# Kernel optimization log

Measured on AMD Instinct MI355X. Metric: run time of the kernel, lower is better.

## Reference

```python
import jax, jax.numpy as jnp
import numpy as np

N, F, E, LIN, C, B = 16384, 500, 128, 128, 10, 4096
P_EDGE = 0.002  # ~32 avg degree


def _l2norm(x):
    # F.normalize(dim=1), eps=1e-12
    n = jnp.linalg.norm(x, axis=1, keepdims=True)
    return x / jnp.maximum(n, 1e-12)


def setup_inputs() -> dict:
    key = jax.random.key(0)
    ks = jax.random.split(key, 10)
    adj = (jax.random.uniform(ks[0], (N, N)) < P_EDGE).astype(jnp.float32)
    idx = jnp.arange(N)
    adj = adj.at[idx, idx].set(1.0)  # self-loops guarantee degree >= 1
    data = jax.random.normal(ks[1], (N, F), dtype=jnp.float32)
    nodes = jax.random.randint(ks[2], (B,), 0, N)
    # Encoder 1: Linear(2F -> E); Encoder 2: Linear(2E -> E); classifier heads
    W1 = jax.random.normal(ks[3], (E, 2 * F), dtype=jnp.float32) * 0.03
    b1 = jnp.zeros((E,), jnp.float32)
    W2 = jax.random.normal(ks[4], (E, 2 * E), dtype=jnp.float32) * 0.06
    b2 = jnp.zeros((E,), jnp.float32)
    Wl1 = jax.random.normal(ks[5], (LIN, E), dtype=jnp.float32) * 0.08
    bl1 = jnp.zeros((LIN,), jnp.float32)
    Wl2 = jax.random.normal(ks[6], (C, LIN), dtype=jnp.float32) * 0.12
    bl2 = jnp.zeros((C,), jnp.float32)
    return {"nodes": nodes, "adj": adj, "data": data,
            "W1": W1, "b1": b1, "W2": W2, "b2": b2,
            "Wl1": Wl1, "bl1": bl1, "Wl2": Wl2, "bl2": bl2}


def reference(nodes, adj, data, W1, b1, W2, b2, Wl1, bl1, Wl2, bl2):
    deg = jnp.sum(adj, axis=1, keepdims=True)  # [N,1]
    # Layer 1 (mean aggregator over full neighbor set): computed for all nodes
    neigh1 = (adj @ data) / deg                               # [N,F]
    h1 = jnp.concatenate([data, neigh1], axis=1)              # [N,2F] (self, neigh)
    H1 = _l2norm(jax.nn.relu(h1 @ W1.T + b1))                 # [N,E]
    # Layer 2: only for the queried node batch
    neigh2 = (adj[nodes] @ H1) / deg[nodes]                   # [B,E]
    h2 = jnp.concatenate([H1[nodes], neigh2], axis=1)         # [B,2E]
    H2 = _l2norm(jax.nn.relu(h2 @ W2.T + b2))                 # [B,E]
    x = H2 @ Wl1.T + bl1                                      # [B,LIN]
    x = x @ Wl2.T + bl2                                       # [B,C]
    return jax.nn.softmax(x, axis=1)
```

## Files before the change

kernel.cpp:

```cpp
#include <hip/hip_runtime.h>
#include <math.h>
#include <stddef.h>

#define N_NODES 16384
#define F_DIM   500
#define KP1     512
#define E_DIM   128
#define C_DIM   10
#define B_DIM   4096
#define MAXDEG  128

typedef __attribute__((ext_vector_type(8))) short short8;
typedef __attribute__((ext_vector_type(4))) float f32x4;

__device__ inline unsigned short f2bf(float f) {
    union { float f; unsigned int u; } v; v.f = f;
    unsigned int u = v.u;
    u += 0x7FFFu + ((u >> 16) & 1u);
    return (unsigned short)(u >> 16);
}

__global__ __launch_bounds__(256) void k_cast_data(const float* __restrict__ src,
                                                   unsigned short* __restrict__ dst) {
    int idx = blockIdx.x * 256 + threadIdx.x;
    int i = idx >> 8, k2 = (idx & 255) * 2;
    unsigned short a = 0, b = 0;
    if (k2 < F_DIM) {
        float2 d = *(const float2*)(src + (size_t)i * F_DIM + k2);
        a = f2bf(d.x); b = f2bf(d.y);
    }
    ushort2 o; o.x = a; o.y = b;
    *(ushort2*)(dst + (size_t)i * KP1 + k2) = o;
}

__global__ __launch_bounds__(256) void k_prep_w1b(const float* __restrict__ W1,
                                                  unsigned short* __restrict__ Wt) {
    int idx = blockIdx.x * 256 + threadIdx.x;
    int n = idx >> 9, k = idx & 511;
    float v = (k < F_DIM) ? W1[(size_t)(n & 127) * 1000 + (n >> 7) * F_DIM + k] : 0.0f;
    Wt[idx] = f2bf(v);
}

__global__ __launch_bounds__(256) void k_prep_w2b(const float* __restrict__ W2,
                                                  unsigned short* __restrict__ Wt) {
    int idx = blockIdx.x * 256 + threadIdx.x;
    int n = idx >> 7, k = idx & 127;
    Wt[idx] = f2bf(W2[(size_t)(n & 127) * 256 + (n >> 7) * 128 + k]);
}

__global__ void k_tp(const float* __restrict__ src, float* __restrict__ dst) {
    __shared__ float tile[32][33];
    const int k0 = blockIdx.x * 32;
    const int e0 = blockIdx.y * 32;
    const int tx = threadIdx.x, ty0 = threadIdx.y;
#pragma unroll
    for (int q = 0; q < 4; ++q) {
        int ty = ty0 + q * 8;
        tile[ty][tx] = src[(size_t)(e0 + ty) * 128 + k0 + tx];
    }
    __syncthreads();
#pragma unroll
    for (int q = 0; q < 4; ++q) {
        int ty = ty0 + q * 8;
        dst[(size_t)(k0 + ty) * 128 + e0 + tx] = tile[tx][ty];
    }
}

__global__ __launch_bounds__(256) void k_gemm_mfma(const unsigned short* __restrict__ A,
                                                   const unsigned short* __restrict__ B,
                                                   int K,
                                                   float* __restrict__ Cout) {
    __shared__ unsigned short sA[32 * 40];
    __shared__ unsigned short sB[256 * 40];
    const int tid  = threadIdx.x;
    const int w    = tid >> 6;
    const int lane = tid & 63;
    const int l16  = lane & 15;
    const int quad = lane >> 4;
    const int blockM = blockIdx.x * 32;
    f32x4 acc[2][4] = {};
    const int nchunks = K >> 5;

    for (int c = 0; c < nchunks; ++c) {
        const int k0 = c << 5;
        if (tid < 128) {
            int row = tid >> 2, cc = tid & 3;
            short8 v = *(const short8*)(A + (size_t)(blockM + row) * K + k0 + cc * 8);
            *(short8*)(sA + row * 40 + cc * 8) = v;
        }
#pragma unroll
        for (int q = 0; q < 4; ++q) {
            int idx = tid + 256 * q;
            int row = idx >> 2, cc = idx & 3;
            short8 v = *(const short8*)(B + (size_t)row * K + k0 + cc * 8);
            *(short8*)(sB + row * 40 + cc * 8) = v;
        }
        __syncthreads();
        short8 af[2], bf[4];
#pragma unroll
        for (int mt = 0; mt < 2; ++mt)
            af[mt] = *(const short8*)(sA + (mt * 16 + l16) * 40 + quad * 8);
#pragma unroll
        for (int nt = 0; nt < 4; ++nt)
            bf[nt] = *(const short8*)(sB + (w * 64 + nt * 16 + l16) * 40 + quad * 8);
#pragma unroll
        for (int mt = 0; mt < 2; ++mt)
#pragma unroll
            for (int nt = 0; nt < 4; ++nt)
                acc[mt][nt] = __builtin_amdgcn_mfma_f32_16x16x32_bf16(af[mt], bf[nt], acc[mt][nt], 0, 0, 0);
        __syncthreads();
    }
#pragma unroll
    for (int mt = 0; mt < 2; ++mt)
#pragma unroll
        for (int nt = 0; nt < 4; ++nt) {
            int col = w * 64 + nt * 16 + l16;
#pragma unroll
            for (int r = 0; r < 4; ++r) {
                int row = blockM + mt * 16 + quad * 4 + r;
                Cout[(size_t)row * 256 + col] = acc[mt][nt][r];
            }
        }
}

__global__ __launch_bounds__(256) void k_agg1(const float* __restrict__ adj,
                                              const float* __restrict__ X,
                                              const float* __restrict__ b1,
                                              unsigned short* __restrict__ H1b,
                                              int* __restrict__ nbr,
                                              int* __restrict__ deg) {
    const int i = blockIdx.x;
    const int t = threadIdx.x;
    const float4* row4 = (const float4*)(adj + (size_t)i * N_NODES);
    __shared__ int s_cnt;
    __shared__ int s_idx[MAXDEG];
    __shared__ float s_part[2][128];
    __shared__ float s_w[2];
    if (t == 0) s_cnt = 0;
    __syncthreads();
    float4 v[16];
#pragma unroll
    for (int p = 0; p < 16; ++p) v[p] = row4[p * 256 + t];
#pragma unroll
    for (int p = 0; p < 16; ++p) {
        int col = p * 1024 + t * 4;
        if (v[p].x != 0.f) { int q = atomicAdd(&s_cnt, 1); if (q < MAXDEG) s_idx[q] = col;     }
        if (v[p].y != 0.f) { int q = atomicAdd(&s_cnt, 1); if (q < MAXDEG) s_idx[q] = col + 1; }
        if (v[p].z != 0.f) { int q = atomicAdd(&s_cnt, 1); if (q < MAXDEG) s_idx[q] = col + 2; }
        if (v[p].w != 0.f) { int q = atomicAdd(&s_cnt, 1); if (q < MAXDEG) s_idx[q] = col + 3; }
    }
    __syncthreads();
    int cnt = s_cnt; if (cnt > MAXDEG) cnt = MAXDEG;
    if (t < cnt) nbr[(size_t)i * MAXDEG + t] = s_idx[t];
    if (t == 0) deg[i] = cnt;
    const float inv = 1.0f / (float)cnt;
    const int col = t & 127;
    const int g = t >> 7;
    float acc = 0.f;
    for (int k = g; k < cnt; k += 2)
        acc += X[(size_t)s_idx[k] * 256 + 128 + col];
    s_part[g][col] = acc;
    __syncthreads();
    float vv = 0.f;
    if (t < 128) {
        float tot = s_part[0][t] + s_part[1][t];
        vv = X[(size_t)i * 256 + t] + tot * inv + b1[t];
        vv = fmaxf(vv, 0.f);
        float s = vv * vv;
#pragma unroll
        for (int off = 32; off > 0; off >>= 1) s += __shfl_down(s, off, 64);
        if ((t & 63) == 0) s_w[t >> 6] = s;
    }
    __syncthreads();
    if (t < 128) {
        float denom = fmaxf(sqrtf(s_w[0] + s_w[1]), 1e-12f);
        H1b[(size_t)i * 128 + t] = f2bf(vv / denom);
    }
}

__global__ __launch_bounds__(128) void k_l2head(const int* __restrict__ nodes,
                                                const int* __restrict__ nbr,
                                                const int* __restrict__ deg,
                                                const float* __restrict__ Y,
                                                const float* __restrict__ b2,
                                                const float* __restrict__ Wl1t,
                                                const float* __restrict__ bl1,
                                                const float* __restrict__ Wl2,
                                                const float* __restrict__ bl2,
                                                float* __restrict__ out) {
    const int b = blockIdx.x;
    const int t = threadIdx.x;
    const int n = nodes[b];
    const int cnt = deg[n];
    __shared__ int s_idx[MAXDEG];
    __shared__ float s_h[128];
    __shared__ float s_x[128];
    __shared__ float s_c[C_DIM];
    __shared__ float s_w[2];
    if (t < cnt) s_idx[t] = nbr[(size_t)n * MAXDEG + t];
    __syncthreads();
    float a0 = 0.f, a1 = 0.f;
    int k = 0;
    for (; k + 1 < cnt; k += 2) {
        a0 += Y[(size_t)s_idx[k]     * 256 + 128 + t];
        a1 += Y[(size_t)s_idx[k + 1] * 256 + 128 + t];
    }
    if (k < cnt) a0 += Y[(size_t)s_idx[k] * 256 + 128 + t];
    float vv = Y[(size_t)n * 256 + t] + (a0 + a1) / (float)cnt + b2[t];
    vv = fmaxf(vv, 0.f);
    float s = vv * vv;
#pragma unroll
    for (int off = 32; off > 0; off >>= 1) s += __shfl_down(s, off, 64);
    if ((t & 63) == 0) s_w[t >> 6] = s;
    __syncthreads();
    float denom = fmaxf(sqrtf(s_w[0] + s_w[1]), 1e-12f);
    s_h[t] = vv / denom;
    __syncthreads();
    float x1 = bl1[t];
#pragma unroll 8
    for (int kk = 0; kk < 128; ++kk)
        x1 += Wl1t[kk * 128 + t] * s_h[kk];
    s_x[t] = x1;
    __syncthreads();
    if (t < C_DIM) {
        float l = bl2[t];
        const float* wr = Wl2 + (size_t)t * 128;
        for (int kk = 0; kk < 128; ++kk) l += wr[kk] * s_x[kk];
        s_c[t] = l;
    }
    __syncthreads();
    if (t < C_DIM) {
        float mx = -1e30f;
        for (int c = 0; c < C_DIM; ++c) mx = fmaxf(mx, s_c[c]);
        float se = 0.f;
        for (int c = 0; c < C_DIM; ++c) se += expf(s_c[c] - mx);
        out[(size_t)b * C_DIM + t] = expf(s_c[t] - mx) / se;
    }
}

extern "C" void kernel_launch(void* const* d_in, const int* in_sizes, int n_in,
                              void* d_out, int out_size, void* d_ws, size_t ws_size,
                              hipStream_t stream) {
    const int*   nodes = (const int*)  d_in[0];
    const float* adj   = (const float*)d_in[1];
    const float* data  = (const float*)d_in[2];
    const float* W1    = (const float*)d_in[3];
    const float* b1    = (const float*)d_in[4];
    const float* W2    = (const float*)d_in[5];
    const float* b2    = (const float*)d_in[6];
    const float* Wl1   = (const float*)d_in[7];
    const float* bl1   = (const float*)d_in[8];
    const float* Wl2   = (const float*)d_in[9];
    const float* bl2   = (const float*)d_in[10];
    float* out = (float*)d_out;

    unsigned short* Ab  = (unsigned short*)d_ws;
    unsigned short* Wt1 = Ab  + (size_t)N_NODES * KP1;
    unsigned short* Wt2 = Wt1 + 256 * KP1;
    unsigned short* H1b = Wt2 + 256 * 128;
    float* Wl1t = (float*)(H1b + (size_t)N_NODES * 128);
    float* X    = Wl1t + 128 * 128;
    float* Y    = X    + (size_t)N_NODES * 256;
    int*   nbr  = (int*)(Y + (size_t)N_NODES * 256);
    int*   deg  = nbr + (size_t)N_NODES * MAXDEG;

    k_cast_data<<<N_NODES, 256, 0, stream>>>(data, Ab);
    k_prep_w1b <<<512, 256, 0, stream>>>(W1, Wt1);
    k_prep_w2b <<<128, 256, 0, stream>>>(W2, Wt2);
    k_tp<<<dim3(4, 4), dim3(32, 8), 0, stream>>>(Wl1, Wl1t);

    k_gemm_mfma<<<N_NODES / 32, 256, 0, stream>>>(Ab, Wt1, KP1, X);
    k_agg1     <<<N_NODES, 256, 0, stream>>>(adj, X, b1, H1b, nbr, deg);

    k_gemm_mfma<<<N_NODES / 32, 256, 0, stream>>>(H1b, Wt2, E_DIM, Y);
    k_l2head   <<<B_DIM, 128, 0, stream>>>(nodes, nbr, deg, Y, b2, Wl1t, bl1, Wl2, bl2, out);
}
```

Before: 1.443 ms.

## Fuse fp32-to-bf16 cast into GEMM and vectorize neighbor gathers

Removes the separate data-cast kernel: the first GEMM now reads the fp32 input directly and converts to bf16 while staging its A tile in shared memory, zero-padding K from 500 up to 512. The neighbor aggregation in k_agg1 and k_l2head now uses 8 groups of 32 lanes, each loading float4 rows, with a shared-memory reduction across groups. k_l2head moves to 256 threads to match. The goal is to avoid a full read-write pass over the input and to expose more memory parallelism in the latency-bound gathers. The cost is extra conversion work inside the GEMM loop, and __syncthreads calls placed inside divergent branches.

```diff
diff --git a/kernel.cpp b/kernel.cpp
--- a/kernel.cpp
+++ b/kernel.cpp
@@ -20,19 +20,6 @@
     return (unsigned short)(u >> 16);
 }
 
-__global__ __launch_bounds__(256) void k_cast_data(const float* __restrict__ src,
-                                                   unsigned short* __restrict__ dst) {
-    int idx = blockIdx.x * 256 + threadIdx.x;
-    int i = idx >> 8, k2 = (idx & 255) * 2;
-    unsigned short a = 0, b = 0;
-    if (k2 < F_DIM) {
-        float2 d = *(const float2*)(src + (size_t)i * F_DIM + k2);
-        a = f2bf(d.x); b = f2bf(d.y);
-    }
-    ushort2 o; o.x = a; o.y = b;
-    *(ushort2*)(dst + (size_t)i * KP1 + k2) = o;
-}
-
 __global__ __launch_bounds__(256) void k_prep_w1b(const float* __restrict__ W1,
                                                   unsigned short* __restrict__ Wt) {
     int idx = blockIdx.x * 256 + threadIdx.x;
@@ -66,9 +53,9 @@
     }
 }
 
-__global__ __launch_bounds__(256) void k_gemm_mfma(const unsigned short* __restrict__ A,
+__global__ __launch_bounds__(256) void k_gemm_mfma(const void* __restrict__ Ap,
+                                                   int Ka, int Kpad, int a_fp32,
                                                    const unsigned short* __restrict__ B,
-                                                   int K,
                                                    float* __restrict__ Cout) {
     __shared__ unsigned short sA[32 * 40];
     __shared__ unsigned short sB[256 * 40];
@@ -79,20 +66,35 @@
     const int quad = lane >> 4;
     const int blockM = blockIdx.x * 32;
     f32x4 acc[2][4] = {};
-    const int nchunks = K >> 5;
+    const int nchunks = Kpad >> 5;
 
     for (int c = 0; c < nchunks; ++c) {
         const int k0 = c << 5;
         if (tid < 128) {
             int row = tid >> 2, cc = tid & 3;
-            short8 v = *(const short8*)(A + (size_t)(blockM + row) * K + k0 + cc * 8);
+            int kbase = k0 + cc * 8;
+            short8 v;
+            if (a_fp32) {
+                const float* Arow = (const float*)Ap + (size_t)(blockM + row) * Ka;
+                float4 f0 = (kbase + 4 <= Ka) ? *(const float4*)(Arow + kbase)
+                                              : make_float4(0.f, 0.f, 0.f, 0.f);
+                float4 f1 = (kbase + 8 <= Ka) ? *(const float4*)(Arow + kbase + 4)
+                                              : make_float4(0.f, 0.f, 0.f, 0.f);
+                v[0] = (short)f2bf(f0.x); v[1] = (short)f2bf(f0.y);
+                v[2] = (short)f2bf(f0.z); v[3] = (short)f2bf(f0.w);
+                v[4] = (short)f2bf(f1.x); v[5] = (short)f2bf(f1.y);
+                v[6] = (short)f2bf(f1.z); v[7] = (short)f2bf(f1.w);
+            } else {
+                v = *(const short8*)((const unsigned short*)Ap +
+                                     (size_t)(blockM + row) * Ka + kbase);
+            }
             *(short8*)(sA + row * 40 + cc * 8) = v;
         }
 #pragma unroll
         for (int q = 0; q < 4; ++q) {
             int idx = tid + 256 * q;
             int row = idx >> 2, cc = idx & 3;
-            short8 v = *(const short8*)(B + (size_t)row * K + k0 + cc * 8);
+            short8 v = *(const short8*)(B + (size_t)row * Kpad + k0 + cc * 8);
             *(short8*)(sB + row * 40 + cc * 8) = v;
         }
         __syncthreads();
@@ -134,7 +136,7 @@
     const float4* row4 = (const float4*)(adj + (size_t)i * N_NODES);
     __shared__ int s_cnt;
     __shared__ int s_idx[MAXDEG];
-    __shared__ float s_part[2][128];
+    __shared__ float s_part[8][128];
     __shared__ float s_w[2];
     if (t == 0) s_cnt = 0;
     __syncthreads();
@@ -154,16 +156,19 @@
     if (t < cnt) nbr[(size_t)i * MAXDEG + t] = s_idx[t];
     if (t == 0) deg[i] = cnt;
     const float inv = 1.0f / (float)cnt;
-    const int col = t & 127;
-    const int g = t >> 7;
-    float acc = 0.f;
-    for (int k = g; k < cnt; k += 2)
-        acc += X[(size_t)s_idx[k] * 256 + 128 + col];
-    s_part[g][col] = acc;
+    const int g = t >> 5, l = t & 31;
+    float4 a4 = make_float4(0.f, 0.f, 0.f, 0.f);
+    for (int k = g; k < cnt; k += 8) {
+        float4 x4 = ((const float4*)(X + (size_t)s_idx[k] * 256 + 128))[l];
+        a4.x += x4.x; a4.y += x4.y; a4.z += x4.z; a4.w += x4.w;
+    }
+    *(float4*)&s_part[g][l * 4] = a4;
     __syncthreads();
     float vv = 0.f;
     if (t < 128) {
-        float tot = s_part[0][t] + s_part[1][t];
+        float tot = 0.f;
+#pragma unroll
+        for (int g2 = 0; g2 < 8; ++g2) tot += s_part[g2][t];
         vv = X[(size_t)i * 256 + t] + tot * inv + b1[t];
         vv = fmaxf(vv, 0.f);
         float s = vv * vv;
@@ -178,7 +183,7 @@
     }
 }
 
-__global__ __launch_bounds__(128) void k_l2head(const int* __restrict__ nodes,
+__global__ __launch_bounds__(256) void k_l2head(const int* __restrict__ nodes,
                                                 const int* __restrict__ nbr,
                                                 const int* __restrict__ deg,
                                                 const float* __restrict__ Y,
@@ -193,40 +198,51 @@
     const int n = nodes[b];
     const int cnt = deg[n];
     __shared__ int s_idx[MAXDEG];
+    __shared__ float s_part[8][128];
     __shared__ float s_h[128];
     __shared__ float s_x[128];
     __shared__ float s_c[C_DIM];
     __shared__ float s_w[2];
     if (t < cnt) s_idx[t] = nbr[(size_t)n * MAXDEG + t];
     __syncthreads();
-    float a0 = 0.f, a1 = 0.f;
-    int k = 0;
-    for (; k + 1 < cnt; k += 2) {
-        a0 += Y[(size_t)s_idx[k]     * 256 + 128 + t];
-        a1 += Y[(size_t)s_idx[k + 1] * 256 + 128 + t];
-    }
-    if (k < cnt) a0 += Y[(size_t)s_idx[k] * 256 + 128 + t];
-    float vv = Y[(size_t)n * 256 + t] + (a0 + a1) / (float)cnt + b2[t];
-    vv = fmaxf(vv, 0.f);
-    float s = vv * vv;
-#pragma unroll
-    for (int off = 32; off > 0; off >>= 1) s += __shfl_down(s, off, 64);
-    if ((t & 63) == 0) s_w[t >> 6] = s;
-    __syncthreads();
-    float denom = fmaxf(sqrtf(s_w[0] + s_w[1]), 1e-12f);
-    s_h[t] = vv / denom;
-    __syncthreads();
-    float x1 = bl1[t];
+    const int g = t >> 5, l = t & 31;
+    float4 a4 = make_float4(0.f, 0.f, 0.f, 0.f);
+    for (int k = g; k < cnt; k += 8) {
+        float4 y4 = ((const float4*)(Y + (size_t)s_idx[k] * 256 + 128))[l];
+        a4.x += y4.x; a4.y += y4.y; a4.z += y4.z; a4.w += y4.w;
+    }
+    *(float4*)&s_part[g][l * 4] = a4;
+    __syncthreads();
+    if (t < 128) {
+        float tot = 0.f;
+#pragma unroll
+        for (int g2 = 0; g2 < 8; ++g2) tot += s_part[g2][t];
+        float vv = Y[(size_t)n * 256 + t] + tot / (float)cnt + b2[t];
+        vv = fmaxf(vv, 0.f);
+        float s = vv * vv;
+#pragma unroll
+        for (int off = 32; off > 0; off >>= 1) s += __shfl_down(s, off, 64);
+        if ((t & 63) == 0) s_w[t >> 6] = s;
+        __syncthreads();
+        float denom = fmaxf(sqrtf(s_w[0] + s_w[1]), 1e-12f);
+        s_h[t] = vv / denom;
+    } else {
+        __syncthreads();
+    }
+    __syncthreads();
+    if (t < 128) {
+        float x1 = bl1[t];
 #pragma unroll 8
-    for (int kk = 0; kk < 128; ++kk)
-        x1 += Wl1t[kk * 128 + t] * s_h[kk];
-    s_x[t] = x1;
+        for (int kk = 0; kk < 128; ++kk)
+            x1 += Wl1t[kk * 128 + t] * s_h[kk];
+        s_x[t] = x1;
+    }
     __syncthreads();
     if (t < C_DIM) {
-        float l = bl2[t];
+        float l2 = bl2[t];
         const float* wr = Wl2 + (size_t)t * 128;
-        for (int kk = 0; kk < 128; ++kk) l += wr[kk] * s_x[kk];
-        s_c[t] = l;
+        for (int kk = 0; kk < 128; ++kk) l2 += wr[kk] * s_x[kk];
+        s_c[t] = l2;
     }
     __syncthreads();
     if (t < C_DIM) {
@@ -254,8 +270,7 @@
     const float* bl2   = (const float*)d_in[10];
     float* out = (float*)d_out;
 
-    unsigned short* Ab  = (unsigned short*)d_ws;
-    unsigned short* Wt1 = Ab  + (size_t)N_NODES * KP1;
+    unsigned short* Wt1 = (unsigned short*)d_ws;
     unsigned short* Wt2 = Wt1 + 256 * KP1;
     unsigned short* H1b = Wt2 + 256 * 128;
     float* Wl1t = (float*)(H1b + (size_t)N_NODES * 128);
@@ -264,14 +279,13 @@
     int*   nbr  = (int*)(Y + (size_t)N_NODES * 256);
     int*   deg  = nbr + (size_t)N_NODES * MAXDEG;
 
-    k_cast_data<<<N_NODES, 256, 0, stream>>>(data, Ab);
     k_prep_w1b <<<512, 256, 0, stream>>>(W1, Wt1);
     k_prep_w2b <<<128, 256, 0, stream>>>(W2, Wt2);
     k_tp<<<dim3(4, 4), dim3(32, 8), 0, stream>>>(Wl1, Wl1t);
 
-    k_gemm_mfma<<<N_NODES / 32, 256, 0, stream>>>(Ab, Wt1, KP1, X);
+    k_gemm_mfma<<<N_NODES / 32, 256, 0, stream>>>(data, F_DIM, KP1, 1, Wt1, X);
     k_agg1     <<<N_NODES, 256, 0, stream>>>(adj, X, b1, H1b, nbr, deg);
 
-    k_gemm_mfma<<<N_NODES / 32, 256, 0, stream>>>(H1b, Wt2, E_DIM, Y);
-    k_l2head   <<<B_DIM, 128, 0, stream>>>(nodes, nbr, deg, Y, b2, Wl1t, bl1, Wl2, bl2, out);
-}
+    k_gemm_mfma<<<N_NODES / 32, 256, 0, stream>>>(H1b, E_DIM, E_DIM, 0, Wt2, Y);
+    k_l2head   <<<B_DIM, 256, 0, stream>>>(nodes, nbr, deg, Y, b2, Wl1t, bl1, Wl2, bl2, out);
+}
```

Measured after the change: 1.424 ms. No clear change (-1.3%).
